# Kernel tuning notes

Measured on AMD Instinct MI355X. Metric: run time of the kernel, lower is better.

The kernel has to match this reference:

```python
import jax, jax.numpy as jnp
import numpy as np


def setup_inputs() -> dict:
    key = jax.random.key(0)
    ks = jax.random.split(key, 5)
    B, D, T, H = 32, 256, 1024, 512
    s = 1.0 / np.sqrt(H)  # PyTorch default init scale
    return {
        "x": jax.random.normal(ks[0], (B, D, T), dtype=jnp.float32),
        "W_ih": jax.random.uniform(ks[1], (4 * H, D), jnp.float32, -s, s),
        "W_hh": jax.random.uniform(ks[2], (4 * H, H), jnp.float32, -s, s),
        "b_ih": jax.random.uniform(ks[3], (4 * H,), jnp.float32, -s, s),
        "b_hh": jax.random.uniform(ks[4], (4 * H,), jnp.float32, -s, s),
    }


def reference(x, W_ih, W_hh, b_ih, b_hh):
    # x: [B, in_dim, T] -> permute to [B, T, in_dim] as in the torch module
    B, D, T = x.shape
    H = W_hh.shape[1]
    xt = jnp.transpose(x, (0, 2, 1))  # [B, T, D]
    # Precompute input contribution for all timesteps in one GEMM: [B, T, 4H]
    gx_all = jnp.einsum("btd,gd->btg", xt, W_ih) + b_ih + b_hh
    gx_all = jnp.swapaxes(gx_all, 0, 1)  # [T, B, 4H] for scan

    def step(carry, gx):
        h, c = carry
        g = gx + h @ W_hh.T  # [B, 4H]
        i, f, gg, o = jnp.split(g, 4, axis=-1)  # PyTorch gate order i,f,g,o
        i = jax.nn.sigmoid(i)
        f = jax.nn.sigmoid(f)
        gg = jnp.tanh(gg)
        o = jax.nn.sigmoid(o)
        c = f * c + i * gg
        h = o * jnp.tanh(c)
        return (h, c), h

    h0 = jnp.zeros((B, H), dtype=x.dtype)
    c0 = jnp.zeros((B, H), dtype=x.dtype)
    _, hs = jax.lax.scan(step, (h0, c0), gx_all)  # hs: [T, B, H]
    out = jnp.transpose(hs, (1, 2, 0))  # [B, H, T] (return_sequences=True)
    return out
```

## Files before the change

### kernel.cpp

```cpp
#include <hip/hip_runtime.h>
#include <math.h>


using short8  = __attribute__((ext_vector_type(8))) short;
using f32x4   = __attribute__((ext_vector_type(4))) float;
using float4v = __attribute__((ext_vector_type(4))) float;
using uint4v  = __attribute__((ext_vector_type(4))) unsigned;

__device__ inline unsigned short f2bf(float f) {
    unsigned u = __float_as_uint(f);
    unsigned r = u + 0x7fffu + ((u >> 16) & 1u);
    return (unsigned short)(r >> 16);
}
__device__ inline float fsig(float x) {
    return __builtin_amdgcn_rcpf(1.0f + __expf(-x));
}
__device__ inline float ftanh(float x) {
    return 2.0f * __builtin_amdgcn_rcpf(1.0f + __expf(-2.0f * x)) - 1.0f;
}

__global__ void zero_flags(unsigned* p) {
    p[blockIdx.x * 256 + threadIdx.x] = 0u;
}

__global__ __launch_bounds__(256) void x_transpose(const float* __restrict__ x,
                                                   unsigned short* __restrict__ xT) {
    __shared__ unsigned short tile[64][65];
    const int tid = threadIdx.x;
    const int t0 = blockIdx.x * 64, d0 = blockIdx.y * 64, b = blockIdx.z;
    for (int p = 0; p < 16; p++) {
        int d = p * 4 + (tid >> 6);
        int t = tid & 63;
        tile[d][t] = f2bf(x[(b * 256 + d0 + d) * 1024 + t0 + t]);
    }
    __syncthreads();
    for (int p = 0; p < 16; p++) {
        int t = p * 4 + (tid >> 6);
        int d = tid & 63;
        xT[(size_t)(t0 + t) * 8192 + b * 256 + d0 + d] = tile[d][t];
    }
}

#define GS 33
#define OS 17

__global__ __launch_bounds__(512) void lstm_rec(const unsigned short* __restrict__ xT,
                                                const float* __restrict__ Wih,
                                                const float* __restrict__ Whh,
                                                const float* __restrict__ bih,
                                                const float* __restrict__ bhh,
                                                float* __restrict__ out,
                                                unsigned* flags,
                                                unsigned* hbuf) {
    __shared__ __align__(16) unsigned short h_lds[16 * 512];
    __shared__ float gates_lds[8 * 16 * GS];
    __shared__ float out_stage[512 * OS];

    const int tid  = threadIdx.x;
    const int wave = tid >> 6;
    const int lane = tid & 63;
    const int quad = lane >> 4, l15 = lane & 15;
    const int l7   = l15 & 7;
    const int group = blockIdx.x & 1;
    const int g     = blockIdx.x >> 1;
    const int gate  = wave >> 1;
    const int kh    = wave & 1;

    short8 whh_frag[2][8];
    short8 wih_frag[2][4];
    float bias_t[2];
    for (int tile = 0; tile < 2; tile++) {
        const int nrow = gate * 512 + g * 32 + tile * 16 + l15;
        for (int ks = 0; ks < 8; ks++) {
            const float* p = &Whh[(size_t)nrow * 512 + kh * 256 + ks * 32 + quad * 8];
            short8 v;
            for (int j = 0; j < 8; j++) v[j] = (short)f2bf(p[j]);
            whh_frag[tile][ks] = v;
        }
        for (int ks = 0; ks < 4; ks++) {
            const float* p = &Wih[(size_t)nrow * 256 + kh * 128 + ks * 32 + quad * 8];
            short8 v;
            for (int j = 0; j < 8; j++) v[j] = (short)f2bf(p[j]);
            wih_frag[tile][ks] = v;
        }
        bias_t[tile] = (kh == 0) ? (bih[nrow] + bhh[nrow]) : 0.0f;
    }

    const int eb = tid >> 5, ek = tid & 31;
    const int e7 = eb & 7;
    const int hidx = g * 32 + ek;
    const bool remote = ((ek >> 1) != g);

    for (int i = tid; i < 16 * 512; i += 512) h_lds[i] = 0;

    const unsigned short* xbase = xT + (size_t)(group * 16 + l15) * 256 + kh * 128 + quad * 8;

    short8 xf[4];
#pragma unroll
    for (int ks = 0; ks < 4; ks++)
        xf[ks] = *(const short8*)(xbase + (size_t)0 * 8192 + ks * 32);

    float c = 0.0f;
    float* out_base = out + ((size_t)(group * 16 + eb) * 512 + hidx) * 1024;
    unsigned* my_flags = flags + group * 512;
    unsigned* hb_base  = hbuf + group * 8192;

    __syncthreads();

    f32x4 acc0 = f32x4{bias_t[0], bias_t[0], bias_t[0], bias_t[0]};
    f32x4 acc1 = f32x4{bias_t[1], bias_t[1], bias_t[1], bias_t[1]};
#pragma unroll
    for (int ks = 0; ks < 4; ks++) {
        acc0 = __builtin_amdgcn_mfma_f32_16x16x32_bf16(xf[ks], wih_frag[0][ks], acc0, 0, 0, 0);
        acc1 = __builtin_amdgcn_mfma_f32_16x16x32_bf16(xf[ks], wih_frag[1][ks], acc1, 0, 0, 0);
    }

    for (int t = 0; t < 1024; t++) {
        if (t + 1 < 1024) {
#pragma unroll
            for (int ks = 0; ks < 4; ks++)
                xf[ks] = *(const short8*)(xbase + (size_t)(t + 1) * 8192 + ks * 32);
        }

#pragma unroll
        for (int ks = 0; ks < 8; ks++) {
            short8 af = *(const short8*)&h_lds[l15 * 512 + (((kh << 5) + (ks << 2) + quad) ^ l7) * 8];
            acc0 = __builtin_amdgcn_mfma_f32_16x16x32_bf16(af, whh_frag[0][ks], acc0, 0, 0, 0);
            acc1 = __builtin_amdgcn_mfma_f32_16x16x32_bf16(af, whh_frag[1][ks], acc1, 0, 0, 0);
        }
        {
            const int prow = (kh * 4 + gate) * 16;
#pragma unroll
            for (int r = 0; r < 4; r++) {
                gates_lds[(prow + quad * 4 + r) * GS + l15]      = acc0[r];
                gates_lds[(prow + quad * 4 + r) * GS + 16 + l15] = acc1[r];
            }
        }
        asm volatile("s_waitcnt lgkmcnt(0)" ::: "memory");
        __builtin_amdgcn_sched_barrier(0);
        __builtin_amdgcn_s_barrier();
        __builtin_amdgcn_sched_barrier(0);

        float iv = gates_lds[(0 * 16 + eb) * GS + ek] + gates_lds[(4 * 16 + eb) * GS + ek];
        float fv = gates_lds[(1 * 16 + eb) * GS + ek] + gates_lds[(5 * 16 + eb) * GS + ek];
        float gv = gates_lds[(2 * 16 + eb) * GS + ek] + gates_lds[(6 * 16 + eb) * GS + ek];
        float ov = gates_lds[(3 * 16 + eb) * GS + ek] + gates_lds[(7 * 16 + eb) * GS + ek];
        iv = fsig(iv); fv = fsig(fv); gv = ftanh(gv); ov = fsig(ov);
        c = fv * c + iv * gv;
        float h = ov * ftanh(c);

        out_stage[tid * OS + (t & 15)] = h;

        unsigned my = f2bf(h);
        {
            int phys = (g * 4 + (ek >> 3)) ^ e7;
            h_lds[eb * 512 + phys * 8 + (ek & 7)] = (unsigned short)my;
        }

        unsigned nb = (unsigned)__shfl_xor((int)my, 1);
        if (t < 1023 && !(ek & 1)) {
            __hip_atomic_store(&hb_base[(t & 1) * 4096 + eb * 256 + g * 16 + (ek >> 1)],
                               my | (nb << 16), __ATOMIC_RELAXED, __HIP_MEMORY_SCOPE_AGENT);
        }

        if ((t & 15) == 15) {
            int t0 = t & ~15;
#pragma unroll
            for (int q = 0; q < 4; q++) {
                float4v v = *(const float4v*)&out_stage[tid * OS + q * 4];
                *(float4v*)&out_base[t0 + q * 4] = v;
            }
        }

        if (t == 1023) break;

        acc0 = f32x4{bias_t[0], bias_t[0], bias_t[0], bias_t[0]};
        acc1 = f32x4{bias_t[1], bias_t[1], bias_t[1], bias_t[1]};
#pragma unroll
        for (int ks = 0; ks < 4; ks++) {
            acc0 = __builtin_amdgcn_mfma_f32_16x16x32_bf16(xf[ks], wih_frag[0][ks], acc0, 0, 0, 0);
            acc1 = __builtin_amdgcn_mfma_f32_16x16x32_bf16(xf[ks], wih_frag[1][ks], acc1, 0, 0, 0);
        }

        asm volatile("s_waitcnt vmcnt(0)" ::: "memory");
        __builtin_amdgcn_sched_barrier(0);
        __builtin_amdgcn_s_barrier();
        __builtin_amdgcn_sched_barrier(0);
        if (tid == 0)
            __hip_atomic_store(&my_flags[g * 32], (unsigned)(t + 1),
                               __ATOMIC_RELAXED, __HIP_MEMORY_SCOPE_AGENT);

        if (wave == 0 && lane < 16) {
            while (__hip_atomic_load(&my_flags[lane * 32], __ATOMIC_RELAXED,
                                     __HIP_MEMORY_SCOPE_AGENT) <= (unsigned)t) { }
        }
        __builtin_amdgcn_s_barrier();
        __builtin_amdgcn_sched_barrier(0);

        if (remote) {
            const unsigned long long* src =
                (const unsigned long long*)&hb_base[(t & 1) * 4096 + eb * 256 + ek * 8];
            unsigned long long v0 = __hip_atomic_load(src + 0, __ATOMIC_RELAXED, __HIP_MEMORY_SCOPE_AGENT);
            unsigned long long v1 = __hip_atomic_load(src + 1, __ATOMIC_RELAXED, __HIP_MEMORY_SCOPE_AGENT);
            unsigned long long v2 = __hip_atomic_load(src + 2, __ATOMIC_RELAXED, __HIP_MEMORY_SCOPE_AGENT);
            unsigned long long v3 = __hip_atomic_load(src + 3, __ATOMIC_RELAXED, __HIP_MEMORY_SCOPE_AGENT);
            int pa = (2 * ek) ^ e7;
            int pb = (2 * ek + 1) ^ e7;
            *(uint4v*)&h_lds[eb * 512 + pa * 8] =
                uint4v{(unsigned)v0, (unsigned)(v0 >> 32), (unsigned)v1, (unsigned)(v1 >> 32)};
            *(uint4v*)&h_lds[eb * 512 + pb * 8] =
                uint4v{(unsigned)v2, (unsigned)(v2 >> 32), (unsigned)v3, (unsigned)(v3 >> 32)};
        }
        asm volatile("s_waitcnt lgkmcnt(0)" ::: "memory");
        __builtin_amdgcn_sched_barrier(0);
        __builtin_amdgcn_s_barrier();
        __builtin_amdgcn_sched_barrier(0);
    }

#pragma unroll
    for (int q = 0; q < 4; q++) {
        float4v v = *(const float4v*)&out_stage[tid * OS + q * 4];
        *(float4v*)&out_base[1008 + q * 4] = v;
    }
}

extern "C" void kernel_launch(void* const* d_in, const int* in_sizes, int n_in,
                              void* d_out, int out_size, void* d_ws, size_t ws_size,
                              hipStream_t stream) {
    (void)in_sizes; (void)n_in; (void)out_size; (void)ws_size;
    const float* x   = (const float*)d_in[0];
    const float* Wih = (const float*)d_in[1];
    const float* Whh = (const float*)d_in[2];
    const float* bih = (const float*)d_in[3];
    const float* bhh = (const float*)d_in[4];
    float* out = (float*)d_out;

    char* ws = (char*)d_ws;
    unsigned short* xT = (unsigned short*)ws;
    unsigned* flags    = (unsigned*)(ws + 16777216);
    unsigned* hbuf     = (unsigned*)(ws + 16777216 + 8192);

    zero_flags<<<8, 256, 0, stream>>>(flags);
    dim3 gT(16, 4, 32);
    x_transpose<<<gT, 256, 0, stream>>>(x, xT);
    lstm_rec<<<32, 512, 0, stream>>>(xT, Wih, Whh, bih, bhh, out, flags, hbuf);
}
```

Baseline: 3.148 ms.

## Replace central flag polling with per-producer polling and fetch in each half-wave

Removes the single wave-0 flag spin and its extra block barrier. Each half-wave now polls the flag of one remote producer block and, once that flag is set, copies only that producer's slice of h into LDS. Remote data can arrive as soon as each producer finishes, without waiting for all 16. The periodic output flush moves after the flag store, so the global writes overlap the wait. The cost is 16 concurrent spinning half-waves hitting the flags, and the remapped hbuf addressing must match the producer layout.

```diff
diff --git a/kernel.cpp b/kernel.cpp
--- a/kernel.cpp
+++ b/kernel.cpp
@@ -89,7 +89,13 @@
     const int eb = tid >> 5, ek = tid & 31;
     const int e7 = eb & 7;
     const int hidx = g * 32 + ek;
-    const bool remote = ((ek >> 1) != g);
+
+    const int c_gp  = wave * 2 + (lane >> 5);
+    const int c_sub = lane & 31;
+    const int c_eb  = c_sub & 15;
+    const int c_gr  = c_sub >> 4;
+    const int c_e7  = c_eb & 7;
+    const bool c_act = (c_gp != g);
 
     for (int i = tid; i < 16 * 512; i += 512) h_lds[i] = 0;
 
@@ -163,6 +169,24 @@
                                my | (nb << 16), __ATOMIC_RELAXED, __HIP_MEMORY_SCOPE_AGENT);
         }
 
+        if (t == 1023) break;
+
+        acc0 = f32x4{bias_t[0], bias_t[0], bias_t[0], bias_t[0]};
+        acc1 = f32x4{bias_t[1], bias_t[1], bias_t[1], bias_t[1]};
+#pragma unroll
+        for (int ks = 0; ks < 4; ks++) {
+            acc0 = __builtin_amdgcn_mfma_f32_16x16x32_bf16(xf[ks], wih_frag[0][ks], acc0, 0, 0, 0);
+            acc1 = __builtin_amdgcn_mfma_f32_16x16x32_bf16(xf[ks], wih_frag[1][ks], acc1, 0, 0, 0);
+        }
+
+        asm volatile("s_waitcnt vmcnt(0)" ::: "memory");
+        __builtin_amdgcn_sched_barrier(0);
+        __builtin_amdgcn_s_barrier();
+        __builtin_amdgcn_sched_barrier(0);
+        if (tid == 0)
+            __hip_atomic_store(&my_flags[g * 32], (unsigned)(t + 1),
+                               __ATOMIC_RELAXED, __HIP_MEMORY_SCOPE_AGENT);
+
         if ((t & 15) == 15) {
             int t0 = t & ~15;
 #pragma unroll
@@ -172,44 +196,22 @@
             }
         }
 
-        if (t == 1023) break;
-
-        acc0 = f32x4{bias_t[0], bias_t[0], bias_t[0], bias_t[0]};
-        acc1 = f32x4{bias_t[1], bias_t[1], bias_t[1], bias_t[1]};
-#pragma unroll
-        for (int ks = 0; ks < 4; ks++) {
-            acc0 = __builtin_amdgcn_mfma_f32_16x16x32_bf16(xf[ks], wih_frag[0][ks], acc0, 0, 0, 0);
-            acc1 = __builtin_amdgcn_mfma_f32_16x16x32_bf16(xf[ks], wih_frag[1][ks], acc1, 0, 0, 0);
-        }
-
-        asm volatile("s_waitcnt vmcnt(0)" ::: "memory");
-        __builtin_amdgcn_sched_barrier(0);
-        __builtin_amdgcn_s_barrier();
-        __builtin_amdgcn_sched_barrier(0);
-        if (tid == 0)
-            __hip_atomic_store(&my_flags[g * 32], (unsigned)(t + 1),
-                               __ATOMIC_RELAXED, __HIP_MEMORY_SCOPE_AGENT);
-
-        if (wave == 0 && lane < 16) {
-            while (__hip_atomic_load(&my_flags[lane * 32], __ATOMIC_RELAXED,
+        if (c_act) {
+            const unsigned* fp = &my_flags[c_gp * 32];
+            while (__hip_atomic_load(fp, __ATOMIC_RELAXED,
                                      __HIP_MEMORY_SCOPE_AGENT) <= (unsigned)t) { }
-        }
-        __builtin_amdgcn_s_barrier();
-        __builtin_amdgcn_sched_barrier(0);
-
-        if (remote) {
-            const unsigned long long* src =
-                (const unsigned long long*)&hb_base[(t & 1) * 4096 + eb * 256 + ek * 8];
-            unsigned long long v0 = __hip_atomic_load(src + 0, __ATOMIC_RELAXED, __HIP_MEMORY_SCOPE_AGENT);
-            unsigned long long v1 = __hip_atomic_load(src + 1, __ATOMIC_RELAXED, __HIP_MEMORY_SCOPE_AGENT);
-            unsigned long long v2 = __hip_atomic_load(src + 2, __ATOMIC_RELAXED, __HIP_MEMORY_SCOPE_AGENT);
-            unsigned long long v3 = __hip_atomic_load(src + 3, __ATOMIC_RELAXED, __HIP_MEMORY_SCOPE_AGENT);
-            int pa = (2 * ek) ^ e7;
-            int pb = (2 * ek + 1) ^ e7;
-            *(uint4v*)&h_lds[eb * 512 + pa * 8] =
-                uint4v{(unsigned)v0, (unsigned)(v0 >> 32), (unsigned)v1, (unsigned)(v1 >> 32)};
-            *(uint4v*)&h_lds[eb * 512 + pb * 8] =
-                uint4v{(unsigned)v2, (unsigned)(v2 >> 32), (unsigned)v3, (unsigned)(v3 >> 32)};
+            const unsigned long long* src = (const unsigned long long*)hb_base +
+                ((t & 1) * 2048 + c_eb * 128 + c_gp * 8);
+            unsigned long long u0 = __hip_atomic_load(src + c_gr * 2 + 0, __ATOMIC_RELAXED, __HIP_MEMORY_SCOPE_AGENT);
+            unsigned long long u1 = __hip_atomic_load(src + c_gr * 2 + 1, __ATOMIC_RELAXED, __HIP_MEMORY_SCOPE_AGENT);
+            unsigned long long u2 = __hip_atomic_load(src + (c_gr + 2) * 2 + 0, __ATOMIC_RELAXED, __HIP_MEMORY_SCOPE_AGENT);
+            unsigned long long u3 = __hip_atomic_load(src + (c_gr + 2) * 2 + 1, __ATOMIC_RELAXED, __HIP_MEMORY_SCOPE_AGENT);
+            int p1 = (c_gp * 4 + c_gr) ^ c_e7;
+            int p2 = (c_gp * 4 + c_gr + 2) ^ c_e7;
+            *(uint4v*)&h_lds[c_eb * 512 + p1 * 8] =
+                uint4v{(unsigned)u0, (unsigned)(u0 >> 32), (unsigned)u1, (unsigned)(u1 >> 32)};
+            *(uint4v*)&h_lds[c_eb * 512 + p2 * 8] =
+                uint4v{(unsigned)u2, (unsigned)(u2 >> 32), (unsigned)u3, (unsigned)(u3 >> 32)};
         }
         asm volatile("s_waitcnt lgkmcnt(0)" ::: "memory");
         __builtin_amdgcn_sched_barrier(0);
```

Result: slower. 3.279 ms (+4.2%).

## Read hidden state directly from global buffer with per-wave flag polling

Applied to the files above, without the earlier changes.

Removes the shared-memory copy of the hidden state. Each wave now polls the producer flags it needs via a ballot loop, then loads its h fragments straight from the global double buffer into MFMA operands. This drops two block-wide barriers and the LDS scatter/gather per timestep, and moves the output flush after the flag publish. In exchange every wave polls separately and does more global loads per step, including reading its own block's slice through the global buffer. The zeroing kernel is enlarged so hbuf starts at zero for step 0.

```diff
diff --git a/kernel.cpp b/kernel.cpp
--- a/kernel.cpp
+++ b/kernel.cpp
@@ -5,7 +5,7 @@
 using short8  = __attribute__((ext_vector_type(8))) short;
 using f32x4   = __attribute__((ext_vector_type(4))) float;
 using float4v = __attribute__((ext_vector_type(4))) float;
-using uint4v  = __attribute__((ext_vector_type(4))) unsigned;
+using ull2    = __attribute__((ext_vector_type(2))) unsigned long long;
 
 __device__ inline unsigned short f2bf(float f) {
     unsigned u = __float_as_uint(f);
@@ -19,7 +19,7 @@
     return 2.0f * __builtin_amdgcn_rcpf(1.0f + __expf(-2.0f * x)) - 1.0f;
 }
 
-__global__ void zero_flags(unsigned* p) {
+__global__ void zero_ws(unsigned* p) {
     p[blockIdx.x * 256 + threadIdx.x] = 0u;
 }
 
@@ -52,7 +52,6 @@
                                                 float* __restrict__ out,
                                                 unsigned* flags,
                                                 unsigned* hbuf) {
-    __shared__ __align__(16) unsigned short h_lds[16 * 512];
     __shared__ float gates_lds[8 * 16 * GS];
     __shared__ float out_stage[512 * OS];
 
@@ -60,7 +59,6 @@
     const int wave = tid >> 6;
     const int lane = tid & 63;
     const int quad = lane >> 4, l15 = lane & 15;
-    const int l7   = l15 & 7;
     const int group = blockIdx.x & 1;
     const int g     = blockIdx.x >> 1;
     const int gate  = wave >> 1;
@@ -87,11 +85,7 @@
     }
 
     const int eb = tid >> 5, ek = tid & 31;
-    const int e7 = eb & 7;
     const int hidx = g * 32 + ek;
-    const bool remote = ((ek >> 1) != g);
-
-    for (int i = tid; i < 16 * 512; i += 512) h_lds[i] = 0;
 
     const unsigned short* xbase = xT + (size_t)(group * 16 + l15) * 256 + kh * 128 + quad * 8;
 
@@ -105,6 +99,11 @@
     unsigned* my_flags = flags + group * 512;
     unsigned* hb_base  = hbuf + group * 8192;
 
+    const unsigned long long* hrow_base =
+        (const unsigned long long*)hb_base + (l15 * 128 + kh * 64 + quad * 2);
+    const unsigned* fpoll = &my_flags[((kh << 3) + (lane & 7)) * 32];
+    const bool poller = (lane < 8);
+
     __syncthreads();
 
     f32x4 acc0 = f32x4{bias_t[0], bias_t[0], bias_t[0], bias_t[0]};
@@ -122,12 +121,35 @@
                 xf[ks] = *(const short8*)(xbase + (size_t)(t + 1) * 8192 + ks * 32);
         }
 
-#pragma unroll
-        for (int ks = 0; ks < 8; ks++) {
-            short8 af = *(const short8*)&h_lds[l15 * 512 + (((kh << 5) + (ks << 2) + quad) ^ l7) * 8];
-            acc0 = __builtin_amdgcn_mfma_f32_16x16x32_bf16(af, whh_frag[0][ks], acc0, 0, 0, 0);
-            acc1 = __builtin_amdgcn_mfma_f32_16x16x32_bf16(af, whh_frag[1][ks], acc1, 0, 0, 0);
-        }
+        {
+            unsigned fv;
+            do {
+                fv = poller ? __hip_atomic_load(fpoll, __ATOMIC_RELAXED,
+                                                __HIP_MEMORY_SCOPE_AGENT)
+                            : ~0u;
+            } while (__ballot(fv >= (unsigned)t) != ~0ull);
+        }
+        __builtin_amdgcn_sched_barrier(0);
+
+        {
+            const unsigned long long* hrow = hrow_base + ((t + 1) & 1) * 2048;
+            unsigned long long u[16];
+#pragma unroll
+            for (int ks = 0; ks < 8; ks++) {
+                u[2 * ks]     = __hip_atomic_load(hrow + (ks << 3),     __ATOMIC_RELAXED, __HIP_MEMORY_SCOPE_AGENT);
+                u[2 * ks + 1] = __hip_atomic_load(hrow + (ks << 3) + 1, __ATOMIC_RELAXED, __HIP_MEMORY_SCOPE_AGENT);
+            }
+#pragma unroll
+            for (int ks = 0; ks < 8; ks++) {
+                ull2 uv;
+                uv[0] = u[2 * ks];
+                uv[1] = u[2 * ks + 1];
+                short8 af = __builtin_bit_cast(short8, uv);
+                acc0 = __builtin_amdgcn_mfma_f32_16x16x32_bf16(af, whh_frag[0][ks], acc0, 0, 0, 0);
+                acc1 = __builtin_amdgcn_mfma_f32_16x16x32_bf16(af, whh_frag[1][ks], acc1, 0, 0, 0);
+            }
+        }
+
         {
             const int prow = (kh * 4 + gate) * 16;
 #pragma unroll
@@ -149,20 +171,33 @@
         c = fv * c + iv * gv;
         float h = ov * ftanh(c);
 
-        out_stage[tid * OS + (t & 15)] = h;
-
         unsigned my = f2bf(h);
-        {
-            int phys = (g * 4 + (ek >> 3)) ^ e7;
-            h_lds[eb * 512 + phys * 8 + (ek & 7)] = (unsigned short)my;
-        }
-
         unsigned nb = (unsigned)__shfl_xor((int)my, 1);
         if (t < 1023 && !(ek & 1)) {
             __hip_atomic_store(&hb_base[(t & 1) * 4096 + eb * 256 + g * 16 + (ek >> 1)],
                                my | (nb << 16), __ATOMIC_RELAXED, __HIP_MEMORY_SCOPE_AGENT);
         }
 
+        out_stage[tid * OS + (t & 15)] = h;
+
+        if (t == 1023) break;
+
+        acc0 = f32x4{bias_t[0], bias_t[0], bias_t[0], bias_t[0]};
+        acc1 = f32x4{bias_t[1], bias_t[1], bias_t[1], bias_t[1]};
+#pragma unroll
+        for (int ks = 0; ks < 4; ks++) {
+            acc0 = __builtin_amdgcn_mfma_f32_16x16x32_bf16(xf[ks], wih_frag[0][ks], acc0, 0, 0, 0);
+            acc1 = __builtin_amdgcn_mfma_f32_16x16x32_bf16(xf[ks], wih_frag[1][ks], acc1, 0, 0, 0);
+        }
+
+        asm volatile("s_waitcnt vmcnt(0)" ::: "memory");
+        __builtin_amdgcn_sched_barrier(0);
+        __builtin_amdgcn_s_barrier();
+        __builtin_amdgcn_sched_barrier(0);
+        if (tid == 0)
+            __hip_atomic_store(&my_flags[g * 32], (unsigned)(t + 1),
+                               __ATOMIC_RELAXED, __HIP_MEMORY_SCOPE_AGENT);
+
         if ((t & 15) == 15) {
             int t0 = t & ~15;
 #pragma unroll
@@ -171,50 +206,6 @@
                 *(float4v*)&out_base[t0 + q * 4] = v;
             }
         }
-
-        if (t == 1023) break;
-
-        acc0 = f32x4{bias_t[0], bias_t[0], bias_t[0], bias_t[0]};
-        acc1 = f32x4{bias_t[1], bias_t[1], bias_t[1], bias_t[1]};
-#pragma unroll
-        for (int ks = 0; ks < 4; ks++) {
-            acc0 = __builtin_amdgcn_mfma_f32_16x16x32_bf16(xf[ks], wih_frag[0][ks], acc0, 0, 0, 0);
-            acc1 = __builtin_amdgcn_mfma_f32_16x16x32_bf16(xf[ks], wih_frag[1][ks], acc1, 0, 0, 0);
-        }
-
-        asm volatile("s_waitcnt vmcnt(0)" ::: "memory");
-        __builtin_amdgcn_sched_barrier(0);
-        __builtin_amdgcn_s_barrier();
-        __builtin_amdgcn_sched_barrier(0);
-        if (tid == 0)
-            __hip_atomic_store(&my_flags[g * 32], (unsigned)(t + 1),
-                               __ATOMIC_RELAXED, __HIP_MEMORY_SCOPE_AGENT);
-
-        if (wave == 0 && lane < 16) {
-            while (__hip_atomic_load(&my_flags[lane * 32], __ATOMIC_RELAXED,
-                                     __HIP_MEMORY_SCOPE_AGENT) <= (unsigned)t) { }
-        }
-        __builtin_amdgcn_s_barrier();
-        __builtin_amdgcn_sched_barrier(0);
-
-        if (remote) {
-            const unsigned long long* src =
-                (const unsigned long long*)&hb_base[(t & 1) * 4096 + eb * 256 + ek * 8];
-            unsigned long long v0 = __hip_atomic_load(src + 0, __ATOMIC_RELAXED, __HIP_MEMORY_SCOPE_AGENT);
-            unsigned long long v1 = __hip_atomic_load(src + 1, __ATOMIC_RELAXED, __HIP_MEMORY_SCOPE_AGENT);
-            unsigned long long v2 = __hip_atomic_load(src + 2, __ATOMIC_RELAXED, __HIP_MEMORY_SCOPE_AGENT);
-            unsigned long long v3 = __hip_atomic_load(src + 3, __ATOMIC_RELAXED, __HIP_MEMORY_SCOPE_AGENT);
-            int pa = (2 * ek) ^ e7;
-            int pb = (2 * ek + 1) ^ e7;
-            *(uint4v*)&h_lds[eb * 512 + pa * 8] =
-                uint4v{(unsigned)v0, (unsigned)(v0 >> 32), (unsigned)v1, (unsigned)(v1 >> 32)};
-            *(uint4v*)&h_lds[eb * 512 + pb * 8] =
-                uint4v{(unsigned)v2, (unsigned)(v2 >> 32), (unsigned)v3, (unsigned)(v3 >> 32)};
-        }
-        asm volatile("s_waitcnt lgkmcnt(0)" ::: "memory");
-        __builtin_amdgcn_sched_barrier(0);
-        __builtin_amdgcn_s_barrier();
-        __builtin_amdgcn_sched_barrier(0);
     }
 
 #pragma unroll
@@ -240,7 +231,7 @@
     unsigned* flags    = (unsigned*)(ws + 16777216);
     unsigned* hbuf     = (unsigned*)(ws + 16777216 + 8192);
 
-    zero_flags<<<8, 256, 0, stream>>>(flags);
+    zero_ws<<<72, 256, 0, stream>>>(flags);
     dim3 gT(16, 4, 32);
     x_transpose<<<gT, 256, 0, stream>>>(x, xT);
     lstm_rec<<<32, 512, 0, stream>>>(xT, Wih, Whh, bih, bhh, out, flags, hbuf);
```

Result: slower. 5.920 ms (+88.1%).
